# Performance work log

Measured on AMD Instinct MI355X. Metric: run time of the kernel, lower is better.

The kernel has to match this reference:

```python
import jax, jax.numpy as jnp
import numpy as np

NOISE_STD = 0.1
TOP_K = 2

def setup_inputs() -> dict:
    key = jax.random.key(0)
    k1, k2, k3, k4 = jax.random.split(key, 4)
    B, S, H = 4, 4096, 2048
    E, SE, NS = 64, 64, 10
    x = jax.random.normal(k1, (B, S, H), dtype=jnp.float32)
    scale_embeddings = jax.random.normal(k2, (NS, SE), dtype=jnp.float32)
    # nn.Linear(H+SE, E, bias=False) weight: [E, H+SE]
    router_w = jax.random.normal(k3, (E, H + SE), dtype=jnp.float32) / np.sqrt(H + SE).astype(np.float32)
    # pre-sampled standard-normal noise (training path), scaled by NOISE_STD inside reference
    noise = jax.random.normal(k4, (B, S, E), dtype=jnp.float32)
    return {"x": x, "scale_embeddings": scale_embeddings, "router_w": router_w,
            "noise": noise, "scale_idx": 3}

def reference(x, scale_embeddings, router_w, noise, scale_idx):
    B, S, _ = x.shape
    # scale_idx is not None branch: lookup one scale embedding, broadcast over tokens
    emb = scale_embeddings[scale_idx]                      # [SE]
    emb = jnp.broadcast_to(emb, (B, S, emb.shape[-1]))     # [B,S,SE]
    x_with_scale = jnp.concatenate([x, emb], axis=-1)      # [B,S,H+SE]
    # router: bias-free linear projection to expert logits
    router_logits = jnp.einsum('bsd,ed->bse', x_with_scale, router_w)
    router_logits = router_logits + noise * NOISE_STD      # training noise injection
    routing_probs = jax.nn.softmax(router_logits, axis=-1)  # [B,S,E]
    routing_weights, selected_experts = jax.lax.top_k(routing_probs, TOP_K)
    routing_weights = routing_weights / routing_weights.sum(axis=-1, keepdims=True)
    # scatter normalized weights into dense dispatch tensor [B,S,E]
    dispatch = (jax.nn.one_hot(selected_experts, routing_probs.shape[-1],
                               dtype=routing_probs.dtype)
                * routing_weights[..., None]).sum(axis=-2)
    return dispatch
```

## Files before the change

kernel.cpp:

```cpp
#include <hip/hip_runtime.h>
#include <hip/hip_bf16.h>
#include <math.h>
#include <stdint.h>


#define H_DIM 2048
#define K_TOTAL 2112
#define E_DIM 64
#define SE_DIM 64
#define TPB 64
#define NBLOCKS 256
#define NSTEP 64
#define WP_TOTAL (NSTEP * 12 * 1024)

typedef float  f32x4 __attribute__((ext_vector_type(4)));
typedef short  s16x8 __attribute__((ext_vector_type(8)));
typedef unsigned int u32x4 __attribute__((ext_vector_type(4)));

__device__ __forceinline__ unsigned short bf16_rne(float f) {
    uint32_t u = __float_as_uint(f);
    return (unsigned short)((u + 0x7FFFu + ((u >> 16) & 1u)) >> 16);
}
__device__ __forceinline__ float bf16_f32(unsigned short h) {
    return __uint_as_float(((uint32_t)h) << 16);
}
__device__ __forceinline__ uint32_t bits_of_bf2(__hip_bfloat162 h) {
    uint32_t u; __builtin_memcpy(&u, &h, 4); return u;
}

__global__ void prep_kernel(const float* __restrict__ W,
                            const float* __restrict__ se,
                            const int* __restrict__ sidx,
                            unsigned short* __restrict__ Wp,
                            float* __restrict__ tail) {
    if (blockIdx.x == 64) {
        int e = threadIdx.x;
        if (e < 64) {
            const float* emb = se + (*sidx) * SE_DIM;
            float t = 0.f;
            for (int j = 0; j < SE_DIM; ++j)
                t = fmaf(emb[j], W[(size_t)e * K_TOTAL + H_DIM + j], t);
            tail[e] = t;
        }
        return;
    }
    int item = blockIdx.x * 256 + threadIdx.x;
    int lane = item & 63;
    int nt   = (item >> 6) & 3;
    int s    = item >> 8;
    int e     = nt * 16 + (lane & 15);
    int kbase = s * 32 + (lane >> 4) * 8;
    const float* wr = W + (size_t)e * K_TOTAL + kbase;
    unsigned short p0[8], p1[8], p2[8];
    #pragma unroll
    for (int j = 0; j < 8; ++j) {
        float v = wr[j];
        unsigned short a0 = bf16_rne(v);
        float r1 = v - bf16_f32(a0);
        unsigned short a1 = bf16_rne(r1);
        float r2 = r1 - bf16_f32(a1);
        p0[j] = a0; p1[j] = a1; p2[j] = bf16_rne(r2);
    }
    size_t rec = (size_t)s * 12 + nt * 3;
    unsigned short* d0 = Wp + (rec + 0) * 512 + lane * 8;
    unsigned short* d1 = Wp + (rec + 1) * 512 + lane * 8;
    unsigned short* d2 = Wp + (rec + 2) * 512 + lane * 8;
    #pragma unroll
    for (int j = 0; j < 8; ++j) { d0[j] = p0[j]; d1[j] = p1[j]; d2[j] = p2[j]; }
}

__device__ __forceinline__ void split3(const float4 fa, const float4 fb,
                                       s16x8& P0, s16x8& P1, s16x8& P2) {
    float f[8] = {fa.x, fa.y, fa.z, fa.w, fb.x, fb.y, fb.z, fb.w};
    uint32_t d0[4], d1[4], d2[4];
    #pragma unroll
    for (int p = 0; p < 4; ++p) {
        float v0 = f[2 * p], v1 = f[2 * p + 1];
        uint32_t u0 = bits_of_bf2(__float22bfloat162_rn(make_float2(v0, v1)));
        float r0 = v0 - __uint_as_float(u0 << 16);
        float r1 = v1 - __uint_as_float(u0 & 0xffff0000u);
        uint32_t u1 = bits_of_bf2(__float22bfloat162_rn(make_float2(r0, r1)));
        float s0 = r0 - __uint_as_float(u1 << 16);
        float s1 = r1 - __uint_as_float(u1 & 0xffff0000u);
        uint32_t u2 = bits_of_bf2(__float22bfloat162_rn(make_float2(s0, s1)));
        d0[p] = u0; d1[p] = u1; d2[p] = u2;
    }
    u32x4 q0 = {d0[0], d0[1], d0[2], d0[3]};
    u32x4 q1 = {d1[0], d1[1], d1[2], d1[3]};
    u32x4 q2 = {d2[0], d2[1], d2[2], d2[3]};
    __builtin_memcpy(&P0, &q0, 16);
    __builtin_memcpy(&P1, &q1, 16);
    __builtin_memcpy(&P2, &q2, 16);
}

__launch_bounds__(256, 1)
__global__ void router_kernel(const float* __restrict__ x,
                              const uint4* __restrict__ wp4,
                              const float* __restrict__ tail_g,
                              const float* __restrict__ noise,
                              float* __restrict__ out) {
    __shared__ float4 res[TPB];

    const int tid  = threadIdx.x;
    const int lane = tid & 63;
    const int wave = __builtin_amdgcn_readfirstlane(tid >> 6);
    const int tok0 = blockIdx.x * TPB;
    const int row  = lane & 15;
    const int quad = lane >> 4;
    const int c    = row;

    const float* aptr = x + (size_t)(tok0 + wave * 16 + row) * H_DIM + quad * 8;

    f32x4 acc[4];
    #pragma unroll
    for (int nt = 0; nt < 4; ++nt) acc[nt] = (f32x4){0.f, 0.f, 0.f, 0.f};

    float4 arA = *(const float4*)(aptr);
    float4 arB = *(const float4*)(aptr + 4);
    uint4 bcur[12];
    #pragma unroll
    for (int q = 0; q < 12; ++q) bcur[q] = wp4[(size_t)q * 64 + lane];

    #pragma unroll 2
    for (int s = 0; s < NSTEP; ++s) {
        float4 nrA, nrB;
        uint4 bnxt[12];
        if (s + 1 < NSTEP) {
            const float* ap = aptr + (size_t)(s + 1) * 32;
            nrA = *(const float4*)(ap);
            nrB = *(const float4*)(ap + 4);
            #pragma unroll
            for (int q = 0; q < 12; ++q)
                bnxt[q] = wp4[((size_t)(s + 1) * 12 + q) * 64 + lane];
        }
        s16x8 A0, A1, A2;
        split3(arA, arB, A0, A1, A2);
        #pragma unroll
        for (int nt = 0; nt < 4; ++nt) {
            s16x8 B0, B1, B2;
            __builtin_memcpy(&B0, &bcur[nt * 3 + 0], 16);
            __builtin_memcpy(&B1, &bcur[nt * 3 + 1], 16);
            __builtin_memcpy(&B2, &bcur[nt * 3 + 2], 16);
            f32x4 a = acc[nt];
            a = __builtin_amdgcn_mfma_f32_16x16x32_bf16(A0, B0, a, 0, 0, 0);
            a = __builtin_amdgcn_mfma_f32_16x16x32_bf16(A0, B1, a, 0, 0, 0);
            a = __builtin_amdgcn_mfma_f32_16x16x32_bf16(A1, B0, a, 0, 0, 0);
            a = __builtin_amdgcn_mfma_f32_16x16x32_bf16(A0, B2, a, 0, 0, 0);
            a = __builtin_amdgcn_mfma_f32_16x16x32_bf16(A1, B1, a, 0, 0, 0);
            a = __builtin_amdgcn_mfma_f32_16x16x32_bf16(A2, B0, a, 0, 0, 0);
            acc[nt] = a;
        }
        arA = nrA; arB = nrB;
        #pragma unroll
        for (int q = 0; q < 12; ++q) bcur[q] = bnxt[q];
    }

    float tl0 = tail_g[c],      tl1 = tail_g[c + 16];
    float tl2 = tail_g[c + 32], tl3 = tail_g[c + 48];
    #pragma unroll
    for (int r = 0; r < 4; ++r) {
        const int tloc = wave * 16 + quad * 4 + r;
        const float* nz = noise + (size_t)(tok0 + tloc) * E_DIM;
        float v0 = acc[0][r] + tl0 + 0.1f * nz[c];
        float v1 = acc[1][r] + tl1 + 0.1f * nz[c + 16];
        float v2 = acc[2][r] + tl2 + 0.1f * nz[c + 32];
        float v3 = acc[3][r] + tl3 + 0.1f * nz[c + 48];
        float V1 = v0; int I1 = c;
        float V2 = -__builtin_inff(); int I2 = c;
        if (v1 > V1) { V2 = V1; I2 = I1; V1 = v1; I1 = c + 16; }
        else if (v1 > V2) { V2 = v1; I2 = c + 16; }
        if (v2 > V1) { V2 = V1; I2 = I1; V1 = v2; I1 = c + 32; }
        else if (v2 > V2) { V2 = v2; I2 = c + 32; }
        if (v3 > V1) { V2 = V1; I2 = I1; V1 = v3; I1 = c + 48; }
        else if (v3 > V2) { V2 = v3; I2 = c + 48; }
        #pragma unroll
        for (int m = 8; m; m >>= 1) {
            float o1 = __shfl_xor(V1, m, 64); int oi1 = __shfl_xor(I1, m, 64);
            float o2 = __shfl_xor(V2, m, 64); int oi2 = __shfl_xor(I2, m, 64);
            if (o1 > V1 || (o1 == V1 && oi1 < I1)) {
                float nv2; int ni2;
                if (V1 > o2 || (V1 == o2 && I1 < oi2)) { nv2 = V1; ni2 = I1; }
                else                                   { nv2 = o2; ni2 = oi2; }
                V1 = o1; I1 = oi1; V2 = nv2; I2 = ni2;
            } else {
                if (o1 > V2 || (o1 == V2 && oi1 < I2)) { V2 = o1; I2 = oi1; }
            }
        }
        if (c == r) {
            float d   = expf(V2 - V1);
            float inv = 1.0f / (1.0f + d);
            res[tloc] = make_float4(inv, __int_as_float(I1), d * inv, __int_as_float(I2));
        }
    }
    __syncthreads();

    float4* outb = (float4*)out + (size_t)blockIdx.x * (TPB * E_DIM / 4);
    #pragma unroll
    for (int pp = 0; pp < 4; ++pp) {
        int p = tid + pp * 256;
        int t = p >> 4, cc = p & 15;
        float4 rr = res[t];
        int ri1 = __float_as_int(rr.y), ri2 = __float_as_int(rr.w);
        int e = cc * 4;
        float4 o;
        o.x = (e + 0 == ri1) ? rr.x : (e + 0 == ri2) ? rr.z : 0.0f;
        o.y = (e + 1 == ri1) ? rr.x : (e + 1 == ri2) ? rr.z : 0.0f;
        o.z = (e + 2 == ri1) ? rr.x : (e + 2 == ri2) ? rr.z : 0.0f;
        o.w = (e + 3 == ri1) ? rr.x : (e + 3 == ri2) ? rr.z : 0.0f;
        outb[p] = o;
    }
}

extern "C" void kernel_launch(void* const* d_in, const int* in_sizes, int n_in,
                              void* d_out, int out_size, void* d_ws, size_t ws_size,
                              hipStream_t stream) {
    const float* x     = (const float*)d_in[0];
    const float* se    = (const float*)d_in[1];
    const float* W     = (const float*)d_in[2];
    const float* noise = (const float*)d_in[3];
    const int*   sidx  = (const int*)d_in[4];
    float* out = (float*)d_out;

    unsigned short* Wp   = (unsigned short*)d_ws;
    float*          tail = (float*)((char*)d_ws + WP_TOTAL);

    hipLaunchKernelGGL(prep_kernel, dim3(65), dim3(256), 0, stream, W, se, sidx, Wp, tail);
    hipLaunchKernelGGL(router_kernel, dim3(NBLOCKS), dim3(256), 0, stream,
                       x, (const uint4*)Wp, tail, noise, out);
}
```

Baseline: 239.2 us.

## Stage packed router weights in LDS and split experts across wave pairs

The packed bf16 weight slices for each K-step are now loaded into a double-buffered LDS tile with global_load_lds and shared by all waves, instead of every wave streaming them into registers itself. Tokens per block drop to 32 so the grid doubles to 512 blocks. Each pair of waves splits the 64 experts in half, which cuts per-wave accumulators and allows two blocks per CU. Partial top-2 candidates from the two expert halves are merged through shared memory. The cost is a block-wide barrier every K-step, an extra merge phase, and less prefetching of the x loads, which now happen only at their point of use.

```diff
diff --git a/kernel.cpp b/kernel.cpp
--- a/kernel.cpp
+++ b/kernel.cpp
@@ -8,14 +8,21 @@
 #define K_TOTAL 2112
 #define E_DIM 64
 #define SE_DIM 64
-#define TPB 64
-#define NBLOCKS 256
 #define NSTEP 64
-#define WP_TOTAL (NSTEP * 12 * 1024)
+#define TPB 32
+#define NBLOCKS (16384 / TPB)
+#define STEP_BYTES (12 * 1024)
+#define WP_TOTAL (NSTEP * STEP_BYTES)
 
 typedef float  f32x4 __attribute__((ext_vector_type(4)));
 typedef short  s16x8 __attribute__((ext_vector_type(8)));
 typedef unsigned int u32x4 __attribute__((ext_vector_type(4)));
+
+typedef uint32_t __attribute__((address_space(1))) gu32_t;
+typedef uint32_t __attribute__((address_space(3))) lu32_t;
+__device__ __forceinline__ void gload_lds16(const void* g, void* l) {
+    __builtin_amdgcn_global_load_lds((const gu32_t*)g, (lu32_t*)l, 16, 0, 0);
+}
 
 __device__ __forceinline__ unsigned short bf16_rne(float f) {
     uint32_t u = __float_as_uint(f);
@@ -93,86 +100,79 @@
     __builtin_memcpy(&P2, &q2, 16);
 }
 
-__launch_bounds__(256, 1)
+__launch_bounds__(256, 2)
 __global__ void router_kernel(const float* __restrict__ x,
-                              const uint4* __restrict__ wp4,
+                              const unsigned char* __restrict__ Wp,
                               const float* __restrict__ tail_g,
                               const float* __restrict__ noise,
                               float* __restrict__ out) {
+    __shared__ __align__(16) unsigned char bb[2][STEP_BYTES];
+    __shared__ float4 cand2[2][TPB];
     __shared__ float4 res[TPB];
 
     const int tid  = threadIdx.x;
     const int lane = tid & 63;
     const int wave = __builtin_amdgcn_readfirstlane(tid >> 6);
+    const int mt   = wave >> 1;
+    const int g    = wave & 1;
     const int tok0 = blockIdx.x * TPB;
     const int row  = lane & 15;
     const int quad = lane >> 4;
     const int c    = row;
 
-    const float* aptr = x + (size_t)(tok0 + wave * 16 + row) * H_DIM + quad * 8;
-
-    f32x4 acc[4];
-    #pragma unroll
-    for (int nt = 0; nt < 4; ++nt) acc[nt] = (f32x4){0.f, 0.f, 0.f, 0.f};
-
-    float4 arA = *(const float4*)(aptr);
-    float4 arB = *(const float4*)(aptr + 4);
-    uint4 bcur[12];
-    #pragma unroll
-    for (int q = 0; q < 12; ++q) bcur[q] = wp4[(size_t)q * 64 + lane];
-
-    #pragma unroll 2
+    const float* aptr = x + (size_t)(tok0 + mt * 16 + row) * H_DIM + quad * 8;
+
+    f32x4 acc0 = {0.f, 0.f, 0.f, 0.f}, acc1 = acc0;
+
+    #pragma unroll
+    for (int i = 0; i < 3; ++i) {
+        int f = tid + i * 256;
+        gload_lds16(Wp + f * 16, &bb[0][f * 16]);
+    }
+
     for (int s = 0; s < NSTEP; ++s) {
-        float4 nrA, nrB;
-        uint4 bnxt[12];
+        __syncthreads();
         if (s + 1 < NSTEP) {
-            const float* ap = aptr + (size_t)(s + 1) * 32;
-            nrA = *(const float4*)(ap);
-            nrB = *(const float4*)(ap + 4);
+            const unsigned char* src = Wp + (size_t)(s + 1) * STEP_BYTES;
             #pragma unroll
-            for (int q = 0; q < 12; ++q)
-                bnxt[q] = wp4[((size_t)(s + 1) * 12 + q) * 64 + lane];
-        }
+            for (int i = 0; i < 3; ++i) {
+                int f = tid + i * 256;
+                gload_lds16(src + f * 16, &bb[(s + 1) & 1][f * 16]);
+            }
+        }
+        const float* ap = aptr + (size_t)s * 32;
+        float4 a0 = *(const float4*)(ap);
+        float4 a1 = *(const float4*)(ap + 4);
         s16x8 A0, A1, A2;
-        split3(arA, arB, A0, A1, A2);
+        split3(a0, a1, A0, A1, A2);
+
+        const unsigned char* base = &bb[s & 1][g * 6144 + lane * 16];
         #pragma unroll
-        for (int nt = 0; nt < 4; ++nt) {
-            s16x8 B0, B1, B2;
-            __builtin_memcpy(&B0, &bcur[nt * 3 + 0], 16);
-            __builtin_memcpy(&B1, &bcur[nt * 3 + 1], 16);
-            __builtin_memcpy(&B2, &bcur[nt * 3 + 2], 16);
-            f32x4 a = acc[nt];
+        for (int nt = 0; nt < 2; ++nt) {
+            s16x8 B0 = *(const s16x8*)(base + (nt * 3 + 0) * 1024);
+            s16x8 B1 = *(const s16x8*)(base + (nt * 3 + 1) * 1024);
+            s16x8 B2 = *(const s16x8*)(base + (nt * 3 + 2) * 1024);
+            f32x4 a = nt ? acc1 : acc0;
             a = __builtin_amdgcn_mfma_f32_16x16x32_bf16(A0, B0, a, 0, 0, 0);
             a = __builtin_amdgcn_mfma_f32_16x16x32_bf16(A0, B1, a, 0, 0, 0);
             a = __builtin_amdgcn_mfma_f32_16x16x32_bf16(A1, B0, a, 0, 0, 0);
             a = __builtin_amdgcn_mfma_f32_16x16x32_bf16(A0, B2, a, 0, 0, 0);
             a = __builtin_amdgcn_mfma_f32_16x16x32_bf16(A1, B1, a, 0, 0, 0);
             a = __builtin_amdgcn_mfma_f32_16x16x32_bf16(A2, B0, a, 0, 0, 0);
-            acc[nt] = a;
-        }
-        arA = nrA; arB = nrB;
-        #pragma unroll
-        for (int q = 0; q < 12; ++q) bcur[q] = bnxt[q];
-    }
-
-    float tl0 = tail_g[c],      tl1 = tail_g[c + 16];
-    float tl2 = tail_g[c + 32], tl3 = tail_g[c + 48];
+            if (nt) acc1 = a; else acc0 = a;
+        }
+    }
+
+    float tl0 = tail_g[g * 32 + c], tl1 = tail_g[g * 32 + 16 + c];
     #pragma unroll
     for (int r = 0; r < 4; ++r) {
-        const int tloc = wave * 16 + quad * 4 + r;
-        const float* nz = noise + (size_t)(tok0 + tloc) * E_DIM;
-        float v0 = acc[0][r] + tl0 + 0.1f * nz[c];
-        float v1 = acc[1][r] + tl1 + 0.1f * nz[c + 16];
-        float v2 = acc[2][r] + tl2 + 0.1f * nz[c + 32];
-        float v3 = acc[3][r] + tl3 + 0.1f * nz[c + 48];
-        float V1 = v0; int I1 = c;
-        float V2 = -__builtin_inff(); int I2 = c;
-        if (v1 > V1) { V2 = V1; I2 = I1; V1 = v1; I1 = c + 16; }
-        else if (v1 > V2) { V2 = v1; I2 = c + 16; }
-        if (v2 > V1) { V2 = V1; I2 = I1; V1 = v2; I1 = c + 32; }
-        else if (v2 > V2) { V2 = v2; I2 = c + 32; }
-        if (v3 > V1) { V2 = V1; I2 = I1; V1 = v3; I1 = c + 48; }
-        else if (v3 > V2) { V2 = v3; I2 = c + 48; }
+        const int tl = mt * 16 + quad * 4 + r;
+        const float* nz = noise + (size_t)(tok0 + tl) * E_DIM + g * 32;
+        float v0 = acc0[r] + tl0 + 0.1f * nz[c];
+        float v1 = acc1[r] + tl1 + 0.1f * nz[16 + c];
+        float V1, V2; int I1, I2;
+        if (v1 > v0) { V1 = v1; I1 = g * 32 + 16 + c; V2 = v0; I2 = g * 32 + c; }
+        else         { V1 = v0; I1 = g * 32 + c;      V2 = v1; I2 = g * 32 + 16 + c; }
         #pragma unroll
         for (int m = 8; m; m >>= 1) {
             float o1 = __shfl_xor(V1, m, 64); int oi1 = __shfl_xor(I1, m, 64);
@@ -186,17 +186,32 @@
                 if (o1 > V2 || (o1 == V2 && oi1 < I2)) { V2 = o1; I2 = oi1; }
             }
         }
-        if (c == r) {
-            float d   = expf(V2 - V1);
-            float inv = 1.0f / (1.0f + d);
-            res[tloc] = make_float4(inv, __int_as_float(I1), d * inv, __int_as_float(I2));
-        }
+        if (c == r)
+            cand2[g][tl] = make_float4(V1, __int_as_float(I1), V2, __int_as_float(I2));
     }
     __syncthreads();
 
+    if (tid < TPB) {
+        float4 c0 = cand2[0][tid];
+        float4 c1 = cand2[1][tid];
+        float V1 = c0.x, V2 = c0.z;
+        int   I1 = __float_as_int(c0.y), I2 = __float_as_int(c0.w);
+        if (c1.x > V1) {
+            if (c1.z > V1) { V2 = c1.z; I2 = __float_as_int(c1.w); }
+            else           { V2 = V1;   I2 = I1; }
+            V1 = c1.x; I1 = __float_as_int(c1.y);
+        } else if (c1.x > V2) {
+            V2 = c1.x; I2 = __float_as_int(c1.y);
+        }
+        float d   = expf(V2 - V1);
+        float inv = 1.0f / (1.0f + d);
+        res[tid] = make_float4(inv, __int_as_float(I1), d * inv, __int_as_float(I2));
+    }
+    __syncthreads();
+
     float4* outb = (float4*)out + (size_t)blockIdx.x * (TPB * E_DIM / 4);
     #pragma unroll
-    for (int pp = 0; pp < 4; ++pp) {
+    for (int pp = 0; pp < 2; ++pp) {
         int p = tid + pp * 256;
         int t = p >> 4, cc = p & 15;
         float4 rr = res[t];
@@ -226,5 +241,5 @@
 
     hipLaunchKernelGGL(prep_kernel, dim3(65), dim3(256), 0, stream, W, se, sidx, Wp, tail);
     hipLaunchKernelGGL(router_kernel, dim3(NBLOCKS), dim3(256), 0, stream,
-                       x, (const uint4*)Wp, tail, noise, out);
-}
+                       x, (const unsigned char*)Wp, tail, noise, out);
+}
```

Measured after the change: 243.1 us. About the same (+1.6%).
